# Performance work log

Measured on AMD Instinct MI355X. Metric: run time of the kernel, lower is better.

## Reference

```python
import jax, jax.numpy as jnp
import numpy as np

A_DIM = 18
HID = 512
LSTM_IN = HID + A_DIM + 1  # 531


def setup_inputs() -> dict:
    key = jax.random.key(0)
    ks = jax.random.split(key, 26)
    T, B = 80, 64
    inp = {}
    inp["o"] = jax.random.randint(ks[0], (T, B, 1, 84, 84), 0, 255, dtype=jnp.int32)
    inp["a"] = jax.random.randint(ks[1], (T, B), 0, A_DIM, dtype=jnp.int32)
    inp["r"] = jax.random.normal(ks[2], (T, B), dtype=jnp.float32)
    inp["done"] = jax.random.randint(ks[3], (T, B), 0, 2, dtype=jnp.int32)
    inp["h0"] = jnp.zeros((B, HID), dtype=jnp.float32)
    inp["c0"] = jnp.zeros((B, HID), dtype=jnp.float32)

    def gw(k, shape, s=0.05):
        return (jax.random.normal(k, shape, dtype=jnp.float32) * s)

    # CNN trunk params (torch Conv2d OIHW layout)
    inp["conv1_w"] = gw(ks[4], (32, 1, 8, 8))
    inp["conv1_b"] = jnp.zeros((32,), jnp.float32)
    inp["conv2_w"] = gw(ks[5], (64, 32, 4, 4))
    inp["conv2_b"] = jnp.zeros((64,), jnp.float32)
    inp["conv3_w"] = gw(ks[6], (64, 64, 3, 3))
    inp["conv3_b"] = jnp.zeros((64,), jnp.float32)
    inp["fc_w"] = gw(ks[7], (HID, 64 * 7 * 7))
    inp["fc_b"] = jnp.zeros((HID,), jnp.float32)
    # LSTM params (torch gate order: i, f, g, o)
    inp["W_ih"] = gw(ks[8], (4 * HID, LSTM_IN))
    inp["W_hh"] = gw(ks[9], (4 * HID, HID))
    inp["b_ih"] = jnp.zeros((4 * HID,), jnp.float32)
    inp["b_hh"] = jnp.zeros((4 * HID,), jnp.float32)
    # Dueling heads
    inp["adv_w1"] = gw(ks[10], (HID, HID))
    inp["adv_b1"] = jnp.zeros((HID,), jnp.float32)
    inp["adv_w2"] = gw(ks[11], (A_DIM, HID))
    inp["adv_b2"] = jnp.zeros((A_DIM,), jnp.float32)
    inp["val_w1"] = gw(ks[12], (HID, HID))
    inp["val_b1"] = jnp.zeros((HID,), jnp.float32)
    inp["val_w2"] = gw(ks[13], (1, HID))
    inp["val_b2"] = jnp.zeros((1,), jnp.float32)
    return inp


def _conv(x, w, b, stride):
    y = jax.lax.conv_general_dilated(
        x, w, (stride, stride), 'VALID',
        dimension_numbers=('NCHW', 'OIHW', 'NCHW'))
    return y + b[None, :, None, None]


def reference(o, a, r, done, h0, c0,
              conv1_w, conv1_b, conv2_w, conv2_b, conv3_w, conv3_b,
              fc_w, fc_b, W_ih, W_hh, b_ih, b_hh,
              adv_w1, adv_b1, adv_w2, adv_b2,
              val_w1, val_b1, val_w2, val_b2):
    T, B = o.shape[0], o.shape[1]
    x = o.reshape(T * B, 1, 84, 84).astype(jnp.float32) / 255.0
    x = jax.nn.relu(_conv(x, conv1_w, conv1_b, 4))   # [TB,32,20,20]
    x = jax.nn.relu(_conv(x, conv2_w, conv2_b, 2))   # [TB,64,9,9]
    x = jax.nn.relu(_conv(x, conv3_w, conv3_b, 1))   # [TB,64,7,7]
    x = x.reshape(T * B, 64 * 7 * 7)
    hidden = jax.nn.relu(x @ fc_w.T + fc_b).reshape(T, B, HID)

    a_one_hot = jax.nn.one_hot(a, A_DIM, dtype=jnp.float32)      # [T,B,A]
    lstm_in = jnp.concatenate([hidden, r[..., None], a_one_hot], axis=-1)  # [T,B,531]
    keep = (1.0 - done.astype(jnp.float32))[..., None]           # [T,B,1]
    bias = b_ih + b_hh

    def step(carry, inp_t):
        h, c = carry
        x_t, m = inp_t
        h = h * m
        c = c * m
        g = x_t @ W_ih.T + h @ W_hh.T + bias   # [B, 4H]
        i, f, gg, oo = jnp.split(g, 4, axis=-1)
        c = jax.nn.sigmoid(f) * c + jax.nn.sigmoid(i) * jnp.tanh(gg)
        h = jax.nn.sigmoid(oo) * jnp.tanh(c)
        return (h, c), h

    (hT, cT), hs = jax.lax.scan(step, (h0, c0), (lstm_in, keep))
    z = hs.reshape(T * B, HID)

    adv = jax.nn.relu(z @ adv_w1.T + adv_b1) @ adv_w2.T + adv_b2  # [TB,A]
    val = jax.nn.relu(z @ val_w1.T + val_b1) @ val_w2.T + val_b2  # [TB,1]
    q = val + (adv - adv.mean(axis=1, keepdims=True))
    return q.reshape(T, B, A_DIM), hT, cT
```

## Files before the change

kernel.cpp:

```cpp
#include <hip/hip_runtime.h>
#include <hip/hip_bf16.h>
#include <stdint.h>

typedef __bf16 bf16;
typedef __bf16 bfrag __attribute__((ext_vector_type(8)));
typedef short s16x8 __attribute__((ext_vector_type(8)));
typedef float f32x4 __attribute__((ext_vector_type(4)));
typedef float f32x16 __attribute__((ext_vector_type(16)));
typedef uint32_t u32x4 __attribute__((ext_vector_type(4)));

#define DEV __device__ __forceinline__

DEV bfrag ldg16(const bf16* p){ return *(const bfrag*)p; }

struct U64x2 { uint64_t a, b; };
DEV bfrag ld2x8(const bf16* p){
  U64x2 t; t.a = *(const uint64_t*)p; t.b = *(const uint64_t*)(p+4);
  return __builtin_bit_cast(bfrag, t);
}

DEV f32x4  mfma16(bfrag a, bfrag b, f32x4  c){ return __builtin_amdgcn_mfma_f32_16x16x32_bf16(a,b,c,0,0,0); }
DEV f32x16 mfma32(bfrag a, bfrag b, f32x16 c){ return __builtin_amdgcn_mfma_f32_32x32x16_bf16(a,b,c,0,0,0); }

DEV f32x16 zero16(){
  f32x16 v;
  for(int i=0;i<16;++i) v[i]=0.f;
  return v;
}
DEV f32x4 zero4(){
  f32x4 v;
  for(int i=0;i<4;++i) v[i]=0.f;
  return v;
}

DEV float sigm(float x){ return 1.0f/(1.0f+__expf(-x)); }
DEV float ftanh(float x){ float e = __expf(2.f*x); return 1.f - 2.f/(e+1.f); }

DEV u32x4 ldcg4(const uint32_t* p){
  u32x4 r;
  asm volatile("global_load_dwordx4 %0, %1, off sc0 sc1" : "=v"(r) : "v"(p));
  return r;
}

DEV uint32_t pk2f(float a, float b){
  bf16 x = (bf16)a, y = (bf16)b;
  return (uint32_t)__builtin_bit_cast(uint16_t,x) | ((uint32_t)__builtin_bit_cast(uint16_t,y)<<16);
}

__global__ __launch_bounds__(256) void k_prep(
    const float* __restrict__ c1w, const float* __restrict__ c2w,
    const float* __restrict__ c3w, const float* __restrict__ fcw,
    const float* __restrict__ Wih, const float* __restrict__ WhhF,
    const float* __restrict__ bih, const float* __restrict__ bhh,
    const float* __restrict__ aw1, const float* __restrict__ aw2,
    const float* __restrict__ vw1, const float* __restrict__ vw2,
    const float* __restrict__ h0, const float* __restrict__ ab1,
    const float* __restrict__ vb1,
    bf16* w1b, bf16* w2r, bf16* w3r, bf16* fcwr, bf16* Wx, bf16* Whh,
    float* biasL, float* Wr, float* Wa, bf16* headw1, float* headb1,
    bf16* w2cat, uint32_t* hcurT)
{
  long i = (long)blockIdx.x*256 + threadIdx.x;
  if (i < 2048){ int co=(int)(i>>6), k=(int)(i&63);
    w1b[i] = (bf16)(c1w[co*64+k]*(1.f/255.f)); return; } i -= 2048;
  if (i < 32768){ int o=(int)(i>>9), k=(int)(i&511);
    int ky=k>>7, kx=(k>>5)&3, ci=k&31;
    w2r[i] = (bf16)c2w[((o*32+ci)*4+ky)*4+kx]; return; } i -= 32768;
  if (i < 36864){ int o=(int)(i/576), k=(int)(i%576);
    int ky=k/192, rem=k-ky*192, kx=rem>>6, ci=rem&63;
    w3r[i] = (bf16)c3w[((o*64+ci)*3+ky)*3+kx]; return; } i -= 36864;
  if (i < 1638400){ int o=(int)(i/3200), k=(int)(i%3200);
    float v = 0.f;
    if (k < 3136){ int y=k/448, rem=k-y*448, x=rem>>6, ci=rem&63;
      v = fcw[o*3136 + ci*49 + y*7 + x]; }
    fcwr[i] = (bf16)v; return; } i -= 1638400;
  if (i < 1048576){ int n=(int)(i>>9), k=(int)(i&511);
    Wx[i] = (bf16)Wih[n*531+k]; return; } i -= 1048576;
  if (i < 1048576){ int n=(int)(i>>9), k=(int)(i&511);
    Whh[i] = (bf16)WhhF[n*512+k]; return; } i -= 1048576;
  if (i < 2048){ biasL[i] = bih[i]+bhh[i]; return; } i -= 2048;
  if (i < 2048){ Wr[i] = Wih[i*531+512]; return; } i -= 2048;
  if (i < 36864){ int j=(int)(i>>11), n=(int)(i&2047);
    Wa[i] = Wih[n*531+513+j]; return; } i -= 36864;
  if (i < 524288){ headw1[i] = (bf16)(i<262144 ? aw1[i] : vw1[i-262144]); return; } i -= 524288;
  if (i < 1024){ headb1[i] = (i<512) ? ab1[i] : vb1[i-512]; return; } i -= 1024;
  if (i < 32768){ int n=(int)(i>>10), k=(int)(i&1023);
    float v = 0.f;
    if (n<18 && k<512) v = aw2[n*512+k];
    else if (n==18 && k>=512) v = vw2[k-512];
    w2cat[i] = (bf16)v; return; } i -= 32768;
  if (i < 32768){
    if (i < 16384){
      int row = (int)(i>>8), wd = (int)(i&255);
      uint32_t pk = pk2f(h0[row*512 + wd*2], h0[row*512 + wd*2 + 1]);
      hcurT[i] = pk & ~0x00010001u;
    } else {
      hcurT[i] = 0x00010000u;
    }
    return;
  }
}

__global__ __launch_bounds__(256,2) void k_conv12(
    const int* __restrict__ o, const bf16* __restrict__ w1b,
    const float* __restrict__ c1b, const bf16* __restrict__ w2r,
    const float* __restrict__ c2b, bf16* __restrict__ act2)
{
  __shared__ bf16 lact[2][14400];
  const int tid = threadIdx.x;
  const int w = tid>>6, l = tid&63;
  const int img = w>>1, h = w&1;
  const long gimg = (long)blockIdx.x*2 + img;
  const int* ip = o + gimg*7056;
  char* lw = (char*)&lact[img][0];
  {
    bfrag bw[4];
    #pragma unroll
    for (int ks=0;ks<4;++ks) bw[ks] = ldg16(w1b + (l&31)*64 + ks*16 + 8*(l>>5));
    const float bias = c1b[l&31];
    for (int mt=h; mt<13; mt+=2){
      f32x16 acc = zero16();
      int m0 = mt*32 + (l&31);
      int p  = m0>399 ? 399 : m0;
      int oy = p/20, ox = p - oy*20;
      #pragma unroll
      for (int ks=0;ks<4;++ks){
        int ky = 2*ks + (l>>5);
        const int* q = ip + (oy*4+ky)*84 + ox*4;
        int4 i0 = *(const int4*)q;
        int4 i1 = *(const int4*)(q+4);
        bfrag a;
        a[0]=(bf16)(float)i0.x; a[1]=(bf16)(float)i0.y;
        a[2]=(bf16)(float)i0.z; a[3]=(bf16)(float)i0.w;
        a[4]=(bf16)(float)i1.x; a[5]=(bf16)(float)i1.y;
        a[6]=(bf16)(float)i1.z; a[7]=(bf16)(float)i1.w;
        acc = mfma32(a, bw[ks], acc);
      }
      #pragma unroll
      for (int r2=0;r2<16;++r2){
        int row = (r2&3) + 8*(r2>>2) + 4*(l>>5);
        int m = mt*32 + row;
        if (m < 400){
          float v = acc[r2] + bias; v = v>0.f ? v : 0.f;
          *(bf16*)(lw + m*72 + (l&31)*2) = (bf16)v;
        }
      }
    }
  }
  __syncthreads();
  {
    f32x16 acc2[3];
    #pragma unroll
    for (int a2=0;a2<3;++a2) acc2[a2]=zero16();
    int pb[3];
    #pragma unroll
    for (int mt=0;mt<3;++mt){
      int m = mt*32 + (l&31); int p = m>80 ? 80 : m;
      int oy = p/9, ox = p - oy*9;
      pb[mt] = (oy*2)*20 + ox*2;
    }
    #pragma unroll 4
    for (int ks=0; ks<32; ++ks){
      int k  = ks*16 + 8*(l>>5);
      int ky = k>>7, kx = (k>>5)&3, ci = k&31;
      bfrag b0 = ldg16(w2r + (32*h + (l&31))*512 + k);
      #pragma unroll
      for (int mt=0; mt<3; ++mt){
        int p2 = pb[mt] + ky*20 + kx;
        bfrag a = ld2x8((const bf16*)(lw + p2*72) + ci);
        acc2[mt] = mfma32(a, b0, acc2[mt]);
      }
    }
    const float bias2 = c2b[32*h + (l&31)];
    #pragma unroll
    for (int mt=0; mt<3; ++mt){
      #pragma unroll
      for (int r2=0;r2<16;++r2){
        int row = (r2&3) + 8*(r2>>2) + 4*(l>>5);
        int m = mt*32 + row;
        if (m < 81){
          float v = acc2[mt][r2] + bias2; v = v>0.f ? v : 0.f;
          act2[gimg*5184 + m*64 + 32*h + (l&31)] = (bf16)v;
        }
      }
    }
  }
}

__global__ __launch_bounds__(256,2) void k_conv3(
    const bf16* __restrict__ act2, const bf16* __restrict__ w3r,
    const float* __restrict__ c3b, bf16* __restrict__ act3)
{
  const int tid=threadIdx.x, w=tid>>6, l=tid&63;
  const long img = (long)blockIdx.x*4 + w;
  const bf16* A = act2 + img*5184;
  f32x16 acc[2][2];
  #pragma unroll
  for(int a2=0;a2<2;++a2){ acc[a2][0]=zero16(); acc[a2][1]=zero16(); }
  #pragma unroll 4
  for (int ks=0; ks<36; ++ks){
    int k  = ks*16 + 8*(l>>5);
    int ky = k/192, rem = k - ky*192, kx = rem>>6, ci = rem&63;
    bfrag b0 = ldg16(w3r + (l&31)*576 + k);
    bfrag b1 = ldg16(w3r + (32+(l&31))*576 + k);
    #pragma unroll
    for (int mt=0; mt<2; ++mt){
      int m = mt*32 + (l&31); int p = m>48 ? 48 : m;
      int oy = p/7, ox = p - oy*7;
      bfrag a = ldg16(A + ((oy+ky)*9 + (ox+kx))*64 + ci);
      acc[mt][0] = mfma32(a, b0, acc[mt][0]);
      acc[mt][1] = mfma32(a, b1, acc[mt][1]);
    }
  }
  const float bias0 = c3b[l&31], bias1 = c3b[32+(l&31)];
  #pragma unroll
  for (int mt=0; mt<2; ++mt){
    #pragma unroll
    for (int r2=0;r2<16;++r2){
      int row = (r2&3) + 8*(r2>>2) + 4*(l>>5);
      int m = mt*32 + row;
      if (m < 50){
        float v0 = 0.f, v1 = 0.f;
        if (m < 49){
          v0 = acc[mt][0][r2] + bias0; v0 = v0>0.f ? v0 : 0.f;
          v1 = acc[mt][1][r2] + bias1; v1 = v1>0.f ? v1 : 0.f;
        }
        act3[img*3200 + m*64 + (l&31)]      = (bf16)v0;
        act3[img*3200 + m*64 + 32 + (l&31)] = (bf16)v1;
      }
    }
  }
}

template<bool RELU, bool OUTBF16>
__global__ __launch_bounds__(256,4) void k_gemm(
    const bf16* __restrict__ A, long lda,
    const bf16* __restrict__ W, long ldb,
    const float* __restrict__ bias,
    float* __restrict__ outF, bf16* __restrict__ outB, long ldo, int K,
    const float* __restrict__ fixR, const int* __restrict__ fixA,
    const float* __restrict__ fixWr, const float* __restrict__ fixWa)
{
  __shared__ bf16 sA[8192];
  char* sb = (char*)sA;
  const int tid=threadIdx.x, w=tid>>6, l=tid&63;
  const int m0 = blockIdx.x*64, n0 = blockIdx.y*128;
  f32x16 acc[2]; acc[0]=zero16(); acc[1]=zero16();
  const int mt = w&1;
  const int rowa = mt*32 + (l&31);
  for (int kc=0; kc<K; kc+=128){
    __syncthreads();
    for (int u = tid; u < 1024; u += 256){
      int row = u>>4, seg = u&15;
      s16x8 v = *(const s16x8*)(A + (long)(m0+row)*lda + kc + seg*8);
      *(s16x8*)(sb + row*256 + ((seg*16) ^ ((row&15)<<4))) = v;
    }
    __syncthreads();
    #pragma unroll
    for (int ks=0; ks<8; ++ks){
      bfrag a = *(const bfrag*)(sb + rowa*256 + ((ks*32 + (l>>5)*16) ^ ((rowa&15)<<4)));
      #pragma unroll
      for (int j=0;j<2;++j){
        int nt = (w>>1)*2 + j;
        bfrag b = ldg16(W + (long)(n0 + nt*32 + (l&31))*ldb + kc + ks*16 + 8*(l>>5));
        acc[j] = mfma32(a, b, acc[j]);
      }
    }
  }
  #pragma unroll
  for (int j=0;j<2;++j){
    int nt = (w>>1)*2 + j;
    int gc = n0 + nt*32 + (l&31);
    float bv = bias ? bias[gc] : 0.f;
    float wrv = fixR ? fixWr[gc] : 0.f;
    #pragma unroll
    for (int r2=0;r2<16;++r2){
      int row = (r2&3) + 8*(r2>>2) + 4*(l>>5);
      long gr = m0 + mt*32 + row;
      float v = acc[j][r2] + bv;
      if (fixR) v += fixR[gr]*wrv + fixWa[(long)fixA[gr]*2048 + gc];
      if (RELU) v = v>0.f ? v : 0.f;
      if (OUTBF16) outB[gr*ldo + gc] = (bf16)v;
      else         outF[gr*ldo + gc] = v;
    }
  }
}

__global__ __launch_bounds__(256,1) void k_lstm(
    const float* __restrict__ G, const int* __restrict__ done,
    const float* __restrict__ c0, const bf16* __restrict__ Whh,
    uint32_t* __restrict__ hcurT, bf16* __restrict__ hseq,
    float* __restrict__ outH, float* __restrict__ outC)
{
  __shared__ bf16 swt[65536];
  __shared__ bf16 sh2[8192];
  __shared__ float sg[4][16][33];
  __shared__ float sc[16][33];
  __shared__ char  sdone[80][16];
  const int tid=threadIdx.x, w=tid>>6, l=tid&63;
  const int blk=blockIdx.x;
  const int grp=(blk&7)>>1, jj=((blk&1)<<3)|(blk>>3);
  const int bb = grp*16, uu = jj*32;

  for (int p=tid; p<512; p+=256){ int m=p>>5, u=p&31; sc[m][u] = c0[(bb+m)*512 + uu + u]; }
  for (int p=tid; p<1280; p+=256){ int t=p>>4, m=p&15; sdone[t][m] = (char)done[t*64 + bb + m]; }

  char* swb = (char*)swt;
  for (int u = tid; u < 8192; u += 256){
    int wg = u>>11, ks2 = (u>>6)&31, ll = u&63;
    int row = uu + (ll&15) + ((ks2&1)<<4);
    int k   = (ks2>>1)*32 + 8*(ll>>4);
    bfrag v = ldg16(Whh + ((long)wg*512 + row)*512 + k);
    *(bfrag*)(swb + ((u*16) ^ ((ks2&7)<<4))) = v;
  }

  char* shb = (char*)sh2;
  const char* wbase = swb + w*32768;
  const int loff = l*16;
  const int srow  = tid>>4;
  const int sci   = tid&15;

  __syncthreads();

  for (int t=0; t<80; ++t){
    float gv0[4], gv1[4];
    {
      const float* Gt = G + ((long)t*64 + bb)*2048 + w*512 + uu;
      #pragma unroll
      for (int r2=0;r2<4;++r2){
        int m2 = (l>>4)*4 + r2;
        gv0[r2] = Gt[(long)m2*2048 + (l&15)];
        gv1[r2] = Gt[(long)m2*2048 + 16 + (l&15)];
      }
    }
    __builtin_amdgcn_sched_barrier(0);
    {
      const uint32_t* hb = hcurT + (size_t)(t&1)*16384 + (size_t)(bb+srow)*256 + sci*16;
      u32x4 hv[4];
      const uint32_t expPat = ((uint32_t)(t&1)) | (((uint32_t)((t>>1)&1))<<16);
      for (;;){
        #pragma unroll
        for (int j2=0;j2<4;++j2) hv[j2] = ldcg4(hb + j2*4);
        asm volatile("s_waitcnt vmcnt(0)" ::: "memory");
        bool ok = true;
        #pragma unroll
        for (int j2=0;j2<4;++j2){
          ok &= ((hv[j2][0]&0x00010001u)==expPat) & ((hv[j2][1]&0x00010001u)==expPat)
              & ((hv[j2][2]&0x00010001u)==expPat) & ((hv[j2][3]&0x00010001u)==expPat);
        }
        if (__all(ok)) break;
        __builtin_amdgcn_s_sleep(1);
      }
      if (sdone[t][srow]){
        #pragma unroll
        for (int j2=0;j2<4;++j2){ u32x4 z = {0,0,0,0}; hv[j2] = z; }
      } else {
        #pragma unroll
        for (int j2=0;j2<4;++j2){
          hv[j2][0] &= ~0x00010001u; hv[j2][1] &= ~0x00010001u;
          hv[j2][2] &= ~0x00010001u; hv[j2][3] &= ~0x00010001u;
        }
      }
      #pragma unroll
      for (int j=0;j<4;++j){
        *(u32x4*)(shb + sci*1024 + ((((srow + 16*j)*16)) ^ ((sci&7)<<4))) = hv[j];
      }
    }
    __syncthreads();
    f32x4 a0e = zero4(), a0o = zero4(), a1e = zero4(), a1o = zero4();
    #pragma unroll
    for (int ks=0; ks<16; ++ks){
      bfrag a  = *(const bfrag*)(shb + ks*1024 + (loff ^ ((ks&7)<<4)));
      bfrag b0 = *(const bfrag*)(wbase + (2*ks)*1024   + (loff ^ (((2*ks)&7)<<4)));
      bfrag b1 = *(const bfrag*)(wbase + (2*ks+1)*1024 + (loff ^ (((2*ks+1)&7)<<4)));
      if (ks & 1){ a0o = mfma16(a, b0, a0o); a1o = mfma16(a, b1, a1o); }
      else       { a0e = mfma16(a, b0, a0e); a1e = mfma16(a, b1, a1e); }
    }
    #pragma unroll
    for (int r2=0;r2<4;++r2){
      int m = (l>>4)*4 + r2;
      sg[w][m][(l&15)]    = a0e[r2] + a0o[r2] + gv0[r2];
      sg[w][m][16+(l&15)] = a1e[r2] + a1o[r2] + gv1[r2];
    }
    __syncthreads();
    {
      int p0 = tid*2; int m = p0>>5, u = p0&31;
      int dn = sdone[t][m];
      float c_0 = dn ? 0.f : sc[m][u];
      float c_1 = dn ? 0.f : sc[m][u+1];
      float i0=sg[0][m][u],   f0=sg[1][m][u],   g0=sg[2][m][u],   o0=sg[3][m][u];
      float i1=sg[0][m][u+1], f1=sg[1][m][u+1], g1=sg[2][m][u+1], o1=sg[3][m][u+1];
      float cn0 = sigm(f0)*c_0 + sigm(i0)*ftanh(g0);
      float cn1 = sigm(f1)*c_1 + sigm(i1)*ftanh(g1);
      float h_0 = sigm(o0)*ftanh(cn0);
      float h_1 = sigm(o1)*ftanh(cn1);
      sc[m][u] = cn0; sc[m][u+1] = cn1;
      uint32_t pk = pk2f(h_0, h_1);
      int p1 = (t+1)&3;
      uint32_t pat = ((uint32_t)(p1&1)) | (((uint32_t)(p1>>1))<<16);
      uint32_t pkT = (pk & ~0x00010001u) | pat;
      __hip_atomic_store(
          hcurT + (size_t)((t+1)&1)*16384 + (size_t)(bb+m)*256 + ((uu+u)>>1),
          pkT, __ATOMIC_RELAXED, __HIP_MEMORY_SCOPE_AGENT);
      *(uint32_t*)(hseq + ((long)t*64 + bb + m)*512 + uu + u) = pk;
      if (t == 79){
        outH[(bb+m)*512 + uu + u]   = h_0;  outH[(bb+m)*512 + uu + u+1] = h_1;
        outC[(bb+m)*512 + uu + u]   = cn0;  outC[(bb+m)*512 + uu + u+1] = cn1;
      }
    }
  }
}

__global__ __launch_bounds__(256) void k_qhead(
    const bf16* __restrict__ zav, const bf16* __restrict__ w2cat,
    const float* __restrict__ ab2, const float* __restrict__ vb2,
    float* __restrict__ q)
{
  __shared__ float sq[4][16][33];
  const int tid=threadIdx.x, w=tid>>6, l=tid&63;
  const int s0 = blockIdx.x*64 + w*16;
  f32x4 acc0 = zero4(), acc1 = zero4();
  const int row = l&15;
  #pragma unroll 4
  for (int ks=0; ks<32; ++ks){
    int k = ks*32 + 8*(l>>4);
    bfrag a  = ldg16(zav + (long)(s0+row)*1024 + k);
    bfrag b0 = ldg16(w2cat + (l&15)*1024 + k);
    bfrag b1 = ldg16(w2cat + (16+(l&15))*1024 + k);
    acc0 = mfma16(a, b0, acc0);
    acc1 = mfma16(a, b1, acc1);
  }
  #pragma unroll
  for (int r2=0;r2<4;++r2){
    int m = (l>>4)*4 + r2;
    sq[w][m][l&15]      = acc0[r2];
    sq[w][m][16+(l&15)] = acc1[r2];
  }
  __syncthreads();
  if (l < 16){
    int s = s0 + l;
    float av[18]; float sum = 0.f;
    #pragma unroll
    for (int j=0;j<18;++j){ av[j] = sq[w][l][j] + ab2[j]; sum += av[j]; }
    float val = sq[w][l][18] + vb2[0];
    float mean = sum * (1.f/18.f);
    #pragma unroll
    for (int j=0;j<18;++j) q[(long)s*18 + j] = val + av[j] - mean;
  }
}

extern "C" void kernel_launch(void* const* d_in, const int* in_sizes, int n_in,
                              void* d_out, int out_size, void* d_ws, size_t ws_size,
                              hipStream_t stream)
{
  (void)in_sizes; (void)n_in; (void)out_size;
  const int*   o_in = (const int*)  d_in[0];
  const int*   a_in = (const int*)  d_in[1];
  const float* r_in = (const float*)d_in[2];
  const int*   done = (const int*)  d_in[3];
  const float* h0   = (const float*)d_in[4];
  const float* c0   = (const float*)d_in[5];
  const float* c1w  = (const float*)d_in[6],  *c1b=(const float*)d_in[7];
  const float* c2w  = (const float*)d_in[8],  *c2b=(const float*)d_in[9];
  const float* c3w  = (const float*)d_in[10], *c3b=(const float*)d_in[11];
  const float* fcw  = (const float*)d_in[12], *fcb=(const float*)d_in[13];
  const float* Wih  = (const float*)d_in[14], *WhhF=(const float*)d_in[15];
  const float* bih  = (const float*)d_in[16], *bhh=(const float*)d_in[17];
  const float* aw1  = (const float*)d_in[18], *ab1=(const float*)d_in[19];
  const float* aw2  = (const float*)d_in[20], *ab2=(const float*)d_in[21];
  const float* vw1  = (const float*)d_in[22], *vb1=(const float*)d_in[23];
  const float* vw2  = (const float*)d_in[24], *vb2=(const float*)d_in[25];

  char* ws = (char*)d_ws;
  size_t off = 0;
  auto alloc = [&](size_t b){ size_t p = off; off = (off + b + 255) & ~(size_t)255; return p; };
  bf16*  act2   = (bf16*) (ws + alloc(53084160));
  bf16*  act3   = (bf16*) (ws + alloc(32768000));
  bf16*  hidden = (bf16*) (ws + alloc(5242880));
  uint32_t* hcurT = (uint32_t*)(ws + alloc(131072));
  bf16*  w1b    = (bf16*) (ws + alloc(4096));
  bf16*  w2r    = (bf16*) (ws + alloc(65536));
  bf16*  w3r    = (bf16*) (ws + alloc(73728));
  bf16*  fcwr   = (bf16*) (ws + alloc(3276800));
  bf16*  Wx     = (bf16*) (ws + alloc(2097152));
  bf16*  Whh    = (bf16*) (ws + alloc(2097152));
  float* biasL  = (float*)(ws + alloc(8192));
  float* Wr     = (float*)(ws + alloc(8192));
  float* Wa     = (float*)(ws + alloc(147456));
  bf16*  headw1 = (bf16*) (ws + alloc(1048576));
  float* headb1 = (float*)(ws + alloc(4096));
  bf16*  w2cat  = (bf16*) (ws + alloc(65536));
  if (off > ws_size) return;

  float* G    = (float*)act2;
  bf16*  hseq = hidden;
  bf16*  zav  = act3;

  float* qout = (float*)d_out;
  float* outH = qout + 92160;
  float* outC = qout + 124928;

  k_prep<<<17340, 256, 0, stream>>>(c1w, c2w, c3w, fcw, Wih, WhhF, bih, bhh,
      aw1, aw2, vw1, vw2, h0, ab1, vb1, w1b, w2r, w3r, fcwr, Wx, Whh,
      biasL, Wr, Wa, headw1, headb1, w2cat, hcurT);

  k_conv12<<<2560, 256, 0, stream>>>(o_in, w1b, c1b, w2r, c2b, act2);
  k_conv3<<<1280, 256, 0, stream>>>(act2, w3r, c3b, act3);
  k_gemm<true,true><<<dim3(80,4), 256, 0, stream>>>(
      act3, 3200, fcwr, 3200, fcb, nullptr, hidden, 512, 3200,
      nullptr, nullptr, nullptr, nullptr);
  k_gemm<false,false><<<dim3(80,16), 256, 0, stream>>>(
      hidden, 512, Wx, 512, biasL, G, nullptr, 2048, 512,
      r_in, a_in, Wr, Wa);

  k_lstm<<<64, 256, 0, stream>>>(G, done, c0, Whh, hcurT, hseq, outH, outC);

  k_gemm<true,true><<<dim3(80,8), 256, 0, stream>>>(
      hseq, 512, headw1, 512, headb1, nullptr, zav, 1024, 512,
      nullptr, nullptr, nullptr, nullptr);
  k_qhead<<<80, 256, 0, stream>>>(zav, w2cat, ab2, vb2, qout);
}
```

Measured before the change: 621.0 us.

## Keep LSTM recurrent weights in registers and stage GEMM A tiles via direct global-to-LDS loads

The LSTM kernel now holds each wave's slice of W_hh in VGPRs (32 bf16x8 fragments) for all 80 timesteps instead of in a 128KB LDS buffer. This removes two LDS reads per MFMA from the serial recurrence critical path. The GEMM A-tile staging now uses global_load_lds to write straight into swizzled LDS, skipping the trip through VGPRs. The costs are higher register pressure in k_lstm (128 extra VGPRs) and an explicit vmcnt wait before the barrier in the GEMM.

```diff
diff --git a/kernel.cpp b/kernel.cpp
--- a/kernel.cpp
+++ b/kernel.cpp
@@ -45,6 +45,12 @@
 DEV uint32_t pk2f(float a, float b){
   bf16 x = (bf16)a, y = (bf16)b;
   return (uint32_t)__builtin_bit_cast(uint16_t,x) | ((uint32_t)__builtin_bit_cast(uint16_t,y)<<16);
+}
+
+DEV void gl_lds16(const bf16* g, void* l){
+  __builtin_amdgcn_global_load_lds(
+      (const __attribute__((address_space(1))) uint32_t*)g,
+      (__attribute__((address_space(3))) uint32_t*)l, 16, 0, 0);
 }
 
 __global__ __launch_bounds__(256) void k_prep(
@@ -250,11 +256,15 @@
   const int rowa = mt*32 + (l&31);
   for (int kc=0; kc<K; kc+=128){
     __syncthreads();
-    for (int u = tid; u < 1024; u += 256){
-      int row = u>>4, seg = u&15;
-      s16x8 v = *(const s16x8*)(A + (long)(m0+row)*lda + kc + seg*8);
-      *(s16x8*)(sb + row*256 + ((seg*16) ^ ((row&15)<<4))) = v;
-    }
+    #pragma unroll
+    for (int j=0;j<4;++j){
+      int idx = j*64 + l;
+      int row = w*16 + (idx>>4);
+      int seg = idx&15;
+      const bf16* gp = A + (long)(m0+row)*lda + kc + (((seg*16) ^ ((row&15)<<4))>>1);
+      gl_lds16(gp, sb + w*4096 + j*1024);
+    }
+    asm volatile("s_waitcnt vmcnt(0)" ::: "memory");
     __syncthreads();
     #pragma unroll
     for (int ks=0; ks<8; ++ks){
@@ -292,7 +302,6 @@
     uint32_t* __restrict__ hcurT, bf16* __restrict__ hseq,
     float* __restrict__ outH, float* __restrict__ outC)
 {
-  __shared__ bf16 swt[65536];
   __shared__ bf16 sh2[8192];
   __shared__ float sg[4][16][33];
   __shared__ float sc[16][33];
@@ -305,17 +314,19 @@
   for (int p=tid; p<512; p+=256){ int m=p>>5, u=p&31; sc[m][u] = c0[(bb+m)*512 + uu + u]; }
   for (int p=tid; p<1280; p+=256){ int t=p>>4, m=p&15; sdone[t][m] = (char)done[t*64 + bb + m]; }
 
-  char* swb = (char*)swt;
-  for (int u = tid; u < 8192; u += 256){
-    int wg = u>>11, ks2 = (u>>6)&31, ll = u&63;
-    int row = uu + (ll&15) + ((ks2&1)<<4);
-    int k   = (ks2>>1)*32 + 8*(ll>>4);
-    bfrag v = ldg16(Whh + ((long)wg*512 + row)*512 + k);
-    *(bfrag*)(swb + ((u*16) ^ ((ks2&7)<<4))) = v;
+  bfrag wb0[16], wb1[16];
+  {
+    const long row0 = (long)w*512 + uu + (l&15);
+    #pragma unroll
+    for (int ks=0; ks<16; ++ks){
+      int k = ks*32 + 8*(l>>4);
+      wb0[ks] = ldg16(Whh + row0*512 + k);
+      wb1[ks] = ldg16(Whh + (row0+16)*512 + k);
+      asm volatile("" : "+v"(wb0[ks]), "+v"(wb1[ks]));
+    }
   }
 
   char* shb = (char*)sh2;
-  const char* wbase = swb + w*32768;
   const int loff = l*16;
   const int srow  = tid>>4;
   const int sci   = tid&15;
@@ -370,11 +381,9 @@
     f32x4 a0e = zero4(), a0o = zero4(), a1e = zero4(), a1o = zero4();
     #pragma unroll
     for (int ks=0; ks<16; ++ks){
-      bfrag a  = *(const bfrag*)(shb + ks*1024 + (loff ^ ((ks&7)<<4)));
-      bfrag b0 = *(const bfrag*)(wbase + (2*ks)*1024   + (loff ^ (((2*ks)&7)<<4)));
-      bfrag b1 = *(const bfrag*)(wbase + (2*ks+1)*1024 + (loff ^ (((2*ks+1)&7)<<4)));
-      if (ks & 1){ a0o = mfma16(a, b0, a0o); a1o = mfma16(a, b1, a1o); }
-      else       { a0e = mfma16(a, b0, a0e); a1e = mfma16(a, b1, a1e); }
+      bfrag a = *(const bfrag*)(shb + ks*1024 + (loff ^ ((ks&7)<<4)));
+      if (ks & 1){ a0o = mfma16(a, wb0[ks], a0o); a1o = mfma16(a, wb1[ks], a1o); }
+      else       { a0e = mfma16(a, wb0[ks], a0e); a1e = mfma16(a, wb1[ks], a1e); }
     }
     #pragma unroll
     for (int r2=0;r2<4;++r2){
```

Result: faster. 602.2 us (-3.0%).
